# Kernel tuning notes

Measured on AMD Instinct MI355X. Metric: run time of the kernel, lower is better.

Reference implementation:

```python
import jax, jax.numpy as jnp
import numpy as np

L, B, E, H2, V = 512, 128, 256, 128, 32000  # seq, batch, embed, hidden per dir, vocab


def setup_inputs() -> dict:
    key = jax.random.key(0)
    ks = jax.random.split(key, 10)
    lengths = jax.random.randint(ks[0], (B,), L // 4, L + 1)
    mask = (jnp.arange(L)[:, None] < lengths[None, :]).astype(jnp.float32)  # [L,B]
    tokens = jax.random.randint(ks[1], (L, B), 0, V)
    tokens = jnp.where(mask > 0, tokens, -1)  # padding value is -1
    emb_table = jax.random.normal(ks[2], (V + 1, E), jnp.float32) * 0.02
    emb_table = emb_table.at[V].set(0.0)  # ignored/pad index embeds to zero
    s = 1.0 / np.sqrt(H2)
    def u(k, shape):
        return jax.random.uniform(k, shape, jnp.float32, -s, s)
    return {
        "tokens": tokens,
        "mask": mask,
        "emb_table": emb_table,
        "W_ih_f": u(ks[3], (4 * H2, E)),
        "W_hh_f": u(ks[4], (4 * H2, H2)),
        "b_f": u(ks[5], (4 * H2,)),  # b_ih + b_hh folded into one bias
        "W_ih_b": u(ks[6], (4 * H2, E)),
        "W_hh_b": u(ks[7], (4 * H2, H2)),
        "b_b": u(ks[8], (4 * H2,)),
    }


def _lstm_scan(xg, W_hh, mask, reverse):
    # xg: [L,B,4*H2] precomputed input projection; mask: [L,B]
    Bv, Hv = xg.shape[1], W_hh.shape[1]

    def step(carry, inp):
        h, c = carry
        g_x, m = inp
        gates = g_x + h @ W_hh.T  # [B,4*H2], torch gate order i,f,g,o
        i, f, g, o = jnp.split(gates, 4, axis=-1)
        c = jax.nn.sigmoid(f) * c + jax.nn.sigmoid(i) * jnp.tanh(g)
        h = jax.nn.sigmoid(o) * jnp.tanh(c)
        m2 = m[:, None]
        h, c = h * m2, c * m2  # mask both states as in the original loop
        return (h, c), h

    init = (jnp.zeros((Bv, Hv), xg.dtype), jnp.zeros((Bv, Hv), xg.dtype))
    _, hs = jax.lax.scan(step, init, (xg, mask), reverse=reverse)
    return hs  # [L,B,H2], in original time order


def reference(tokens, mask, emb_table, W_ih_f, W_hh_f, b_f, W_ih_b, W_hh_b, b_b):
    pad_id = emb_table.shape[0] - 1
    q = jnp.where(tokens == -1, pad_id, tokens)  # q = data + (data==-1)*(V+1)
    x = emb_table[q]  # [L,B,E]
    # dropout p=0.0 -> identity
    xg_f = jnp.einsum('lbe,ge->lbg', x, W_ih_f) + b_f  # hoist input matmuls
    xg_b = jnp.einsum('lbe,ge->lbg', x, W_ih_b) + b_b
    h_f = _lstm_scan(xg_f, W_hh_f, mask, reverse=False)
    h_b = _lstm_scan(xg_b, W_hh_b, mask, reverse=True)
    return jnp.concatenate([h_f, h_b], axis=-1)  # [L,B,hidden_size]
```

## Files before the change

### kernel.cpp

```cpp
#include <hip/hip_runtime.h>
#include <cmath>

#define LSEQ   512
#define BATCH  128
#define EDIM   256
#define HDIM   128
#define GDIM   512
#define NVOC   32001
#define PADROW 32000

typedef __attribute__((ext_vector_type(8))) _Float16 half8;
typedef __attribute__((ext_vector_type(4))) _Float16 half4;
typedef __attribute__((ext_vector_type(4))) float    f32x4;

#define LO_SCALE 4096.f
#define LO_INV   (1.f / 4096.f)

__global__ __launch_bounds__(512) void g_gemm(
    const float* __restrict__ emb,
    const float* __restrict__ Wf, const float* __restrict__ Wb,
    const float* __restrict__ bf, const float* __restrict__ bb,
    float* __restrict__ G)
{
    const int nb  = blockIdx.x & 7;
    const int dir = blockIdx.x >> 3;
    const int mb  = blockIdx.y;
    const float* W    = dir ? Wb : Wf;
    const float* bias = dir ? bb : bf;
    float* Gd = G + (size_t)dir * NVOC * GDIM;

    __shared__ _Float16 Ah[128][136], Al[128][136];
    __shared__ _Float16 Bh[64][136],  Bl[64][136];

    const int tid  = threadIdx.x;
    const int m0   = mb * 128;
    const int n0   = nb * 64;
    const int w    = tid >> 6;
    const int lane = tid & 63;
    const int lr   = lane & 15;
    const int lg   = lane >> 4;

    f32x4 acc_m[4], acc_x[4];
    #pragma unroll
    for (int nt = 0; nt < 4; ++nt) {
        acc_m[nt] = (f32x4){0.f, 0.f, 0.f, 0.f};
        acc_x[nt] = (f32x4){0.f, 0.f, 0.f, 0.f};
    }

    for (int kh = 0; kh < 2; ++kh) {
        __syncthreads();
        #pragma unroll
        for (int it = 0; it < 8; ++it) {
            int ch  = tid + 512 * it;
            int row = ch >> 5;
            int c4  = ch & 31;
            int v   = m0 + row; if (v > PADROW) v = PADROW;
            f32x4 s = *(const f32x4*)(emb + (size_t)v * EDIM + kh * 128 + c4 * 4);
            half4 hv, lv;
            #pragma unroll
            for (int jj = 0; jj < 4; ++jj) {
                _Float16 hi = (_Float16)s[jj];
                hv[jj] = hi;
                lv[jj] = (_Float16)((s[jj] - (float)hi) * LO_SCALE);
            }
            *(half4*)&Ah[row][c4 * 4] = hv;
            *(half4*)&Al[row][c4 * 4] = lv;
        }
        #pragma unroll
        for (int it = 0; it < 4; ++it) {
            int ch  = tid + 512 * it;
            int row = ch >> 5;
            int c4  = ch & 31;
            f32x4 s = *(const f32x4*)(W + (size_t)(n0 + row) * EDIM + kh * 128 + c4 * 4);
            half4 hv, lv;
            #pragma unroll
            for (int jj = 0; jj < 4; ++jj) {
                _Float16 hi = (_Float16)s[jj];
                hv[jj] = hi;
                lv[jj] = (_Float16)((s[jj] - (float)hi) * LO_SCALE);
            }
            *(half4*)&Bh[row][c4 * 4] = hv;
            *(half4*)&Bl[row][c4 * 4] = lv;
        }
        __syncthreads();

        #pragma unroll
        for (int ks = 0; ks < 4; ++ks) {
            half8 ah = *(const half8*)&Ah[16 * w + lr][32 * ks + 8 * lg];
            half8 al = *(const half8*)&Al[16 * w + lr][32 * ks + 8 * lg];
            #pragma unroll
            for (int nt = 0; nt < 4; ++nt) {
                half8 bh = *(const half8*)&Bh[16 * nt + lr][32 * ks + 8 * lg];
                half8 bl = *(const half8*)&Bl[16 * nt + lr][32 * ks + 8 * lg];
                acc_m[nt] = __builtin_amdgcn_mfma_f32_16x16x32_f16(ah, bh, acc_m[nt], 0, 0, 0);
                acc_x[nt] = __builtin_amdgcn_mfma_f32_16x16x32_f16(al, bh, acc_x[nt], 0, 0, 0);
                acc_x[nt] = __builtin_amdgcn_mfma_f32_16x16x32_f16(ah, bl, acc_x[nt], 0, 0, 0);
            }
        }
    }

    #pragma unroll
    for (int nt = 0; nt < 4; ++nt) {
        int ng = n0 + nt * 16 + lr;
        float bv = bias[ng];
        #pragma unroll
        for (int r = 0; r < 4; ++r) {
            int v = m0 + 16 * w + 4 * lg + r;
            if (v < NVOC)
                Gd[(size_t)v * GDIM + ng] = acc_m[nt][r] + acc_x[nt][r] * LO_INV + bv;
        }
    }
}

__device__ __forceinline__ float sigm(float x) {
    return __builtin_amdgcn_rcpf(1.f + __builtin_amdgcn_exp2f(-1.4426950408889634f * x));
}
__device__ __forceinline__ float tanh_fast(float x) {
    return 1.f - 2.f * __builtin_amdgcn_rcpf(1.f + __builtin_amdgcn_exp2f(2.8853900817779268f * x));
}

__global__ __launch_bounds__(512) void lstm_scan_v2(
    const int*   __restrict__ tokens,
    const float* __restrict__ Whh_f, const float* __restrict__ Whh_b,
    const float* __restrict__ G,
    float* __restrict__ out)
{
    const int dir = blockIdx.x >> 7;
    const int b   = blockIdx.x & 127;
    const float* Whh = dir ? Whh_b : Whh_f;
    const float* Gd  = G + (size_t)dir * NVOC * GDIM;

    __shared__ int   tok[LSEQ];
    __shared__ float hbuf[2][HDIM];

    const int tid  = threadIdx.x;
    const int w    = tid >> 6;
    const int lane = tid & 63;
    const int lr   = lane & 15;
    const int lg   = lane >> 4;
    const int j    = 16 * w + lr;

    tok[tid] = tokens[(size_t)tid * BATCH + b];
    if (tid < 2 * HDIM) ((float*)hbuf)[tid] = 0.f;

    float wreg[4][8][4];
    int   offs[8];
    #pragma unroll
    for (int i = 0; i < 8; ++i) {
        int c   = (i + 2 * lg) & 7;
        offs[i] = 128 * lg + 16 * c;
        #pragma unroll
        for (int gt = 0; gt < 4; ++gt) {
            f32x4 v = *(const f32x4*)(Whh + (size_t)(128 * gt + j) * HDIM + 32 * lg + 4 * c);
            wreg[gt][i][0] = v.x; wreg[gt][i][1] = v.y;
            wreg[gt][i][2] = v.z; wreg[gt][i][3] = v.w;
        }
    }
    __syncthreads();

    auto rowof = [&](int t) -> int {
        int l  = dir ? (LSEQ - 1 - t) : t;
        int tk = tok[l];
        return (tk < 0) ? PADROW : tk;
    };

    float xgA[4], xgB[4];
    {
        size_t ro = (size_t)rowof(0) * GDIM;
        #pragma unroll
        for (int gt = 0; gt < 4; ++gt) xgA[gt] = Gd[ro + 128 * gt + j];
    }

    float c = 0.f;
    const size_t out_base = (size_t)b * 256 + (size_t)dir * HDIM + j;

    auto step = [&](int t, float (&xgc)[4], float (&xgn)[4]) {
        const int l = dir ? (LSEQ - 1 - t) : t;

        if (t + 1 < LSEQ) {
            size_t ro = (size_t)rowof(t + 1) * GDIM;
            #pragma unroll
            for (int gt = 0; gt < 4; ++gt) xgn[gt] = Gd[ro + 128 * gt + j];
        }

        const char* hB = (const char*)&hbuf[t & 1][0];
        f32x4 hc[8];
        #pragma unroll
        for (int i = 0; i < 8; ++i) hc[i] = *(const f32x4*)(hB + offs[i]);

        float a0 = 0.f, a1 = 0.f, a2 = 0.f, a3 = 0.f;
        #pragma unroll
        for (int i = 0; i < 8; ++i) {
            #pragma unroll
            for (int m = 0; m < 4; ++m) {
                a0 = fmaf(hc[i][m], wreg[0][i][m], a0);
                a1 = fmaf(hc[i][m], wreg[1][i][m], a1);
                a2 = fmaf(hc[i][m], wreg[2][i][m], a2);
                a3 = fmaf(hc[i][m], wreg[3][i][m], a3);
            }
        }
        a0 += __shfl_xor(a0, 16); a0 += __shfl_xor(a0, 32);
        a1 += __shfl_xor(a1, 16); a1 += __shfl_xor(a1, 32);
        a2 += __shfl_xor(a2, 16); a2 += __shfl_xor(a2, 32);
        a3 += __shfl_xor(a3, 16); a3 += __shfl_xor(a3, 32);

        float iv = sigm(a0 + xgc[0]);
        float fv = sigm(a1 + xgc[1]);
        float gv = tanh_fast(a2 + xgc[2]);
        float ov = sigm(a3 + xgc[3]);
        c = fv * c + iv * gv;
        float h = ov * tanh_fast(c);
        if (tok[l] < 0) { c = 0.f; h = 0.f; }

        if (lg == 0) {
            hbuf[(t + 1) & 1][j] = h;
            out[(size_t)l * (BATCH * 256) + out_base] = h;
        }
        asm volatile("s_waitcnt lgkmcnt(0)" ::: "memory");
        __builtin_amdgcn_s_barrier();
    };

    for (int t = 0; t < LSEQ; t += 2) {
        step(t,     xgA, xgB);
        step(t + 1, xgB, xgA);
    }
}

extern "C" void kernel_launch(void* const* d_in, const int* in_sizes, int n_in,
                              void* d_out, int out_size, void* d_ws, size_t ws_size,
                              hipStream_t stream) {
    const int*   tokens = (const int*)  d_in[0];
    const float* emb    = (const float*)d_in[2];
    const float* W_ih_f = (const float*)d_in[3];
    const float* W_hh_f = (const float*)d_in[4];
    const float* b_f    = (const float*)d_in[5];
    const float* W_ih_b = (const float*)d_in[6];
    const float* W_hh_b = (const float*)d_in[7];
    const float* b_b    = (const float*)d_in[8];

    float* G = (float*)d_ws;

    g_gemm<<<dim3(16, 251), 512, 0, stream>>>(emb, W_ih_f, W_ih_b, b_f, b_b, G);
    lstm_scan_v2<<<256, 512, 0, stream>>>(tokens, W_hh_f, W_hh_b, G,
                                          (float*)d_out);
}
```

Before: 539.5 us.

## Use split-fp16 MFMA for recurrent h·W_hh matvec in LSTM scan

Replaces the per-step scalar FMA matvec and its cross-lane shuffle reductions with MFMA 16x16x32 fp16 instructions. Precision is kept by splitting both h and W_hh into hi and scaled-lo fp16 parts. W_hh is kept pinned in AGPRs and h is stored in LDS as hi/lo fp16 halves. Each step now issues 48 MFMAs on a 1-row vector, so most of the tile is wasted work and the step depends on MFMA latency. Launch bounds now request two blocks per CU.

After: 654.2 us. 21.3% more time.

```diff
diff --git a/kernel.cpp b/kernel.cpp
--- a/kernel.cpp
+++ b/kernel.cpp
@@ -119,7 +119,7 @@
     return 1.f - 2.f * __builtin_amdgcn_rcpf(1.f + __builtin_amdgcn_exp2f(2.8853900817779268f * x));
 }
 
-__global__ __launch_bounds__(512) void lstm_scan_v2(
+__global__ __launch_bounds__(512, 2) void lstm_scan_v8(
     const int*   __restrict__ tokens,
     const float* __restrict__ Whh_f, const float* __restrict__ Whh_b,
     const float* __restrict__ G,
@@ -130,8 +130,9 @@
     const float* Whh = dir ? Whh_b : Whh_f;
     const float* Gd  = G + (size_t)dir * NVOC * GDIM;
 
-    __shared__ int   tok[LSEQ];
-    __shared__ float hbuf[2][HDIM];
+    __shared__ int      tok[LSEQ];
+    __shared__ _Float16 hh[2][HDIM];
+    __shared__ _Float16 hl[2][HDIM];
 
     const int tid  = threadIdx.x;
     const int w    = tid >> 6;
@@ -141,21 +142,37 @@
     const int j    = 16 * w + lr;
 
     tok[tid] = tokens[(size_t)tid * BATCH + b];
-    if (tid < 2 * HDIM) ((float*)hbuf)[tid] = 0.f;
-
-    float wreg[4][8][4];
-    int   offs[8];
-    #pragma unroll
-    for (int i = 0; i < 8; ++i) {
-        int c   = (i + 2 * lg) & 7;
-        offs[i] = 128 * lg + 16 * c;
-        #pragma unroll
-        for (int gt = 0; gt < 4; ++gt) {
-            f32x4 v = *(const f32x4*)(Whh + (size_t)(128 * gt + j) * HDIM + 32 * lg + 4 * c);
-            wreg[gt][i][0] = v.x; wreg[gt][i][1] = v.y;
-            wreg[gt][i][2] = v.z; wreg[gt][i][3] = v.w;
-        }
-    }
+    if (tid < HDIM) {
+        hh[0][tid] = (_Float16)0.f; hh[1][tid] = (_Float16)0.f;
+        hl[0][tid] = (_Float16)0.f; hl[1][tid] = (_Float16)0.f;
+    }
+
+    half8 wh[4][4], wl[4][4];
+    #pragma unroll
+    for (int tt = 0; tt < 4; ++tt) {
+        const float* wrow = Whh + (size_t)(128 * tt + j) * HDIM;
+        #pragma unroll
+        for (int ks = 0; ks < 4; ++ks) {
+            const float* wp = wrow + 32 * ks + 8 * lg;
+            half8 hv, lv;
+            #pragma unroll
+            for (int jj = 0; jj < 8; ++jj) {
+                float x = wp[jj];
+                _Float16 hi = (_Float16)x;
+                hv[jj] = hi;
+                lv[jj] = (_Float16)((x - (float)hi) * LO_SCALE);
+            }
+            wh[tt][ks] = hv;
+            wl[tt][ks] = lv;
+        }
+    }
+    #pragma unroll
+    for (int tt = 0; tt < 4; ++tt)
+        #pragma unroll
+        for (int ks = 0; ks < 4; ++ks) {
+            asm volatile("" : "+a"(wh[tt][ks]));
+            asm volatile("" : "+a"(wl[tt][ks]));
+        }
     __syncthreads();
 
     auto rowof = [&](int t) -> int {
@@ -183,38 +200,52 @@
             for (int gt = 0; gt < 4; ++gt) xgn[gt] = Gd[ro + 128 * gt + j];
         }
 
-        const char* hB = (const char*)&hbuf[t & 1][0];
-        f32x4 hc[8];
-        #pragma unroll
-        for (int i = 0; i < 8; ++i) hc[i] = *(const f32x4*)(hB + offs[i]);
-
-        float a0 = 0.f, a1 = 0.f, a2 = 0.f, a3 = 0.f;
-        #pragma unroll
-        for (int i = 0; i < 8; ++i) {
-            #pragma unroll
-            for (int m = 0; m < 4; ++m) {
-                a0 = fmaf(hc[i][m], wreg[0][i][m], a0);
-                a1 = fmaf(hc[i][m], wreg[1][i][m], a1);
-                a2 = fmaf(hc[i][m], wreg[2][i][m], a2);
-                a3 = fmaf(hc[i][m], wreg[3][i][m], a3);
-            }
-        }
-        a0 += __shfl_xor(a0, 16); a0 += __shfl_xor(a0, 32);
-        a1 += __shfl_xor(a1, 16); a1 += __shfl_xor(a1, 32);
-        a2 += __shfl_xor(a2, 16); a2 += __shfl_xor(a2, 32);
-        a3 += __shfl_xor(a3, 16); a3 += __shfl_xor(a3, 32);
-
-        float iv = sigm(a0 + xgc[0]);
-        float fv = sigm(a1 + xgc[1]);
-        float gv = tanh_fast(a2 + xgc[2]);
-        float ov = sigm(a3 + xgc[3]);
+        const _Float16* hbH = hh[t & 1];
+        const _Float16* hbL = hl[t & 1];
+        half8 ah[4], al[4];
+        #pragma unroll
+        for (int ks = 0; ks < 4; ++ks) {
+            ah[ks] = *(const half8*)&hbH[32 * ks + 8 * lg];
+            al[ks] = *(const half8*)&hbL[32 * ks + 8 * lg];
+        }
+
+        f32x4 am[4], ax[4];
+        #pragma unroll
+        for (int tt = 0; tt < 4; ++tt) {
+            am[tt] = (f32x4){0.f, 0.f, 0.f, 0.f};
+            ax[tt] = (f32x4){0.f, 0.f, 0.f, 0.f};
+        }
+        #pragma unroll
+        for (int ks = 0; ks < 4; ++ks) {
+            #pragma unroll
+            for (int tt = 0; tt < 4; ++tt)
+                am[tt] = __builtin_amdgcn_mfma_f32_16x16x32_f16(ah[ks], wh[tt][ks], am[tt], 0, 0, 0);
+            #pragma unroll
+            for (int tt = 0; tt < 4; ++tt)
+                ax[tt] = __builtin_amdgcn_mfma_f32_16x16x32_f16(al[ks], wh[tt][ks], ax[tt], 0, 0, 0);
+            #pragma unroll
+            for (int tt = 0; tt < 4; ++tt)
+                ax[tt] = __builtin_amdgcn_mfma_f32_16x16x32_f16(ah[ks], wl[tt][ks], ax[tt], 0, 0, 0);
+        }
+
+        float g0 = am[0][0] + ax[0][0] * LO_INV + xgc[0];
+        float g1 = am[1][0] + ax[1][0] * LO_INV + xgc[1];
+        float g2 = am[2][0] + ax[2][0] * LO_INV + xgc[2];
+        float g3 = am[3][0] + ax[3][0] * LO_INV + xgc[3];
+
+        float iv = sigm(g0);
+        float fv = sigm(g1);
+        float gv = tanh_fast(g2);
+        float ov = sigm(g3);
         c = fv * c + iv * gv;
         float h = ov * tanh_fast(c);
         if (tok[l] < 0) { c = 0.f; h = 0.f; }
 
         if (lg == 0) {
-            hbuf[(t + 1) & 1][j] = h;
             out[(size_t)l * (BATCH * 256) + out_base] = h;
+            _Float16 hhi = (_Float16)h;
+            hh[(t + 1) & 1][j] = hhi;
+            hl[(t + 1) & 1][j] = (_Float16)((h - (float)hhi) * LO_SCALE);
         }
         asm volatile("s_waitcnt lgkmcnt(0)" ::: "memory");
         __builtin_amdgcn_s_barrier();
@@ -241,6 +272,6 @@
     float* G = (float*)d_ws;
 
     g_gemm<<<dim3(16, 251), 512, 0, stream>>>(emb, W_ih_f, W_ih_b, b_f, b_b, G);
-    lstm_scan_v2<<<256, 512, 0, stream>>>(tokens, W_hh_f, W_hh_b, G,
+    lstm_scan_v8<<<256, 512, 0, stream>>>(tokens, W_hh_f, W_hh_b, G,
                                           (float*)d_out);
 }
```
